# Kernel optimization log

Hardware: AMD Instinct MI355X
Metric: run time of the kernel (lower is better)

The kernel has to match this reference:

```python
import jax, jax.numpy as jnp
import numpy as np

N = 100000
E = 1600000
IN = 128
HID = 128
OUT = 64


def sage_conv(x, src, dst, deg_inv, W_l, b_l, W_r):
    # PyG SAGEConv (mean aggr): out = lin_l(mean_{j in N(i)} x_j) + lin_r(x_i)
    msgs = x[src]                                   # [E, F] gather
    agg = jax.ops.segment_sum(msgs, dst, num_segments=N)  # [N, F]
    agg = agg * deg_inv[:, None]                    # mean
    return agg @ W_l + b_l + x @ W_r


def setup_inputs() -> dict:
    key = jax.random.key(0)
    ks = jax.random.split(key, 9)
    x = jax.random.normal(ks[0], (N, IN), dtype=jnp.float32)
    edge_index = jax.random.randint(ks[1], (2, E), 0, N, dtype=jnp.int64)
    s = 1.0 / np.sqrt(IN)
    W1l = jax.random.uniform(ks[2], (IN, HID), jnp.float32, -s, s)
    b1 = jax.random.uniform(ks[3], (HID,), jnp.float32, -s, s)
    W1r = jax.random.uniform(ks[4], (IN, HID), jnp.float32, -s, s)
    s2 = 1.0 / np.sqrt(HID)
    W2l = jax.random.uniform(ks[5], (HID, HID), jnp.float32, -s2, s2)
    b2 = jax.random.uniform(ks[6], (HID,), jnp.float32, -s2, s2)
    W2r = jax.random.uniform(ks[7], (HID, HID), jnp.float32, -s2, s2)
    kl1, kl2 = jax.random.split(ks[8])
    Wlin = jax.random.uniform(kl1, (HID, OUT), jnp.float32, -s2, s2)
    blin = jax.random.uniform(kl2, (OUT,), jnp.float32, -s2, s2)
    return {"x": x, "edge_index": edge_index, "W1l": W1l, "b1": b1, "W1r": W1r,
            "W2l": W2l, "b2": b2, "W2r": W2r, "Wlin": Wlin, "blin": blin}


def reference(x, edge_index, W1l, b1, W1r, W2l, b2, W2r, Wlin, blin):
    src, dst = edge_index[0], edge_index[1]
    deg = jax.ops.segment_sum(jnp.ones((E,), jnp.float32), dst, num_segments=N)
    deg_inv = 1.0 / jnp.maximum(deg, 1.0)
    h = sage_conv(x, src, dst, deg_inv, W1l, b1, W1r)
    h = jax.nn.relu(h)
    # dropout: training=False -> identity
    h2 = sage_conv(h, src, dst, deg_inv, W2l, b2, W2r)
    h = jax.nn.relu(h + h2)
    return h @ Wlin + blin
```

## Files before the change

kernel.cpp:

```cpp
#include <hip/hip_runtime.h>
#include <hip/hip_bf16.h>
#include <cstdint>

#define NND 100000
#define NED 1600000
#define FIN 128
#define FOUT 64

#define NBLK 512
#define EPB (NED / NBLK)
#define NBUCK 256
#define BSH 9
#define BNODES 512
#define HTN (NBUCK * NBLK)

typedef __bf16 bf16x8 __attribute__((ext_vector_type(8)));
typedef float f32x4 __attribute__((ext_vector_type(4)));

static __device__ inline unsigned short f2bf(float f) {
    unsigned int u = __builtin_bit_cast(unsigned int, f);
    unsigned int r = (u + 0x7fffu + ((u >> 16) & 1u)) >> 16;
    return (unsigned short)r;
}
static __device__ inline float bflo(unsigned int v) {
    return __builtin_bit_cast(float, v << 16);
}
static __device__ inline float bfhi(unsigned int v) {
    return __builtin_bit_cast(float, v & 0xffff0000u);
}
static __device__ inline float bf1(unsigned short u) {
    return __builtin_bit_cast(float, (unsigned int)u << 16);
}

static __device__ inline void pack_one(const float* __restrict__ W,
                                       unsigned short* __restrict__ out,
                                       int NTtot, int c_local, int nt,
                                       int chunkOff, int ncols, int lane) {
    int k = c_local * 32 + (lane >> 4) * 8;
    int n = nt * 16 + (lane & 15);
    unsigned short t[8];
#pragma unroll
    for (int j = 0; j < 8; j++) t[j] = f2bf(W[(size_t)(k + j) * ncols + n]);
    uint4 u;
    u.x = t[0] | ((unsigned)t[1] << 16);
    u.y = t[2] | ((unsigned)t[3] << 16);
    u.z = t[4] | ((unsigned)t[5] << 16);
    u.w = t[6] | ((unsigned)t[7] << 16);
    *(uint4*)&out[((size_t)((c_local + chunkOff) * NTtot + nt) * 64 + lane) * 8] = u;
}

__global__ __launch_bounds__(256) void k_hist_cast(
        const int* __restrict__ dst, int* __restrict__ histT,
        const float* __restrict__ x, unsigned int* __restrict__ xb,
        const float* W1l, const float* W1r, const float* W2l,
        const float* W2r, const float* Wlin,
        unsigned short* p1, unsigned short* p2, unsigned short* ph) {
    __shared__ int hist[NBUCK];
    const int tid = threadIdx.x, blk = blockIdx.x;
    hist[tid] = 0;
    __syncthreads();
    const int e0 = blk * EPB, e1 = e0 + EPB;
    for (int i = e0 + tid; i < e1; i += 256)
        atomicAdd(&hist[dst[i] >> BSH], 1);
    __syncthreads();
    histT[tid * NBLK + blk] = hist[tid];
    if (blk < 144 && tid < 64) {
        int b = blk, lane = tid;
        if (b < 32)       pack_one(W1l, p1, 8, b >> 3, b & 7, 0, 128, lane);
        else if (b < 64)  { b -= 32; pack_one(W1r, p1, 8, b >> 3, b & 7, 4, 128, lane); }
        else if (b < 96)  { b -= 64; pack_one(W2l, p2, 8, b >> 3, b & 7, 0, 128, lane); }
        else if (b < 128) { b -= 96; pack_one(W2r, p2, 8, b >> 3, b & 7, 4, 128, lane); }
        else              { b -= 128; pack_one(Wlin, ph, 4, b >> 2, b & 3, 0, 64, lane); }
    }
    const int total2 = NND * 64;
    for (int i = blk * 256 + tid; i < total2; i += NBLK * 256) {
        float2 v = ((const float2*)x)[i];
        xb[i] = (unsigned int)f2bf(v.x) | ((unsigned int)f2bf(v.y) << 16);
    }
}

__global__ __launch_bounds__(1024) void g_scan1(const int* __restrict__ in,
                                                int* __restrict__ psum, int n) {
    __shared__ int red[1024];
    int tid = threadIdx.x;
    int i = blockIdx.x * 1024 + tid;
    red[tid] = (i < n) ? in[i] : 0;
    __syncthreads();
#pragma unroll
    for (int off = 512; off > 0; off >>= 1) {
        if (tid < off) red[tid] += red[tid + off];
        __syncthreads();
    }
    if (tid == 0) psum[blockIdx.x] = red[0];
}

__global__ __launch_bounds__(128) void g_scan2(int* __restrict__ psum, int nb) {
    int tid = threadIdx.x;
    int d = (tid < nb) ? psum[tid] : 0;
    int v = d;
#pragma unroll
    for (int off = 1; off < 64; off <<= 1) {
        int u = __shfl_up(v, off, 64);
        if ((tid & 63) >= off) v += u;
    }
    __shared__ int ws[2];
    if ((tid & 63) == 63) ws[tid >> 6] = v;
    __syncthreads();
    int base = (tid >= 64) ? ws[0] : 0;
    if (tid < nb) psum[tid] = base + v - d;
}

__global__ __launch_bounds__(1024) void g_scan3(const int* __restrict__ in,
                                                const int* __restrict__ psum,
                                                int* __restrict__ out, int n) {
    int tid = threadIdx.x;
    int i = blockIdx.x * 1024 + tid;
    int d = (i < n) ? in[i] : 0;
    int v = d;
#pragma unroll
    for (int off = 1; off < 64; off <<= 1) {
        int u = __shfl_up(v, off, 64);
        if ((tid & 63) >= off) v += u;
    }
    __shared__ int wsum[16];
    int wid = tid >> 6;
    if ((tid & 63) == 63) wsum[wid] = v;
    __syncthreads();
    if (tid < 16) {
        int w = wsum[tid];
#pragma unroll
        for (int off = 1; off < 16; off <<= 1) {
            int u = __shfl_up(w, off, 64);
            if (tid >= off) w += u;
        }
        wsum[tid] = w;
    }
    __syncthreads();
    int base = psum[blockIdx.x] + (wid ? wsum[wid - 1] : 0);
    if (i < n) out[i] = base + v - d;
}

__global__ __launch_bounds__(256) void k_scatter(const int* __restrict__ src,
                                                 const int* __restrict__ dst,
                                                 const int* __restrict__ sh,
                                                 uint2* __restrict__ eS) {
    __shared__ int cur[NBUCK];
    const int tid = threadIdx.x, blk = blockIdx.x;
    cur[tid] = sh[tid * NBLK + blk];
    __syncthreads();
    const int e0 = blk * EPB, e1 = e0 + EPB;
    for (int i = e0 + tid; i < e1; i += 256) {
        int d = dst[i];
        int pos = atomicAdd(&cur[d >> BSH], 1);
        eS[pos] = make_uint2((unsigned)src[i], (unsigned)(d & (BNODES - 1)));
    }
}

__global__ __launch_bounds__(1024) void k_bucket(const uint2* __restrict__ eS,
                                                 const int* __restrict__ sh,
                                                 int* __restrict__ csr,
                                                 int* __restrict__ offs,
                                                 float* __restrict__ dinv, int n) {
    __shared__ int cnt[BNODES];
    __shared__ int loc[BNODES];
    const int b = blockIdx.x, tid = threadIdx.x;
    const int base = sh[b * NBLK];
    const int end = (b == NBUCK - 1) ? NED : sh[(b + 1) * NBLK];
    if (tid < BNODES) cnt[tid] = 0;
    __syncthreads();
    for (int i = base + tid; i < end; i += 1024)
        atomicAdd(&cnt[eS[i].y], 1);
    __syncthreads();
    if (tid < BNODES) loc[tid] = cnt[tid];
    __syncthreads();
#pragma unroll
    for (int off = 1; off < BNODES; off <<= 1) {
        int v = 0;
        if (tid < BNODES && tid >= off) v = loc[tid - off];
        __syncthreads();
        if (tid < BNODES) loc[tid] += v;
        __syncthreads();
    }
    int node = b * BNODES + tid;
    int myExcl = 0;
    if (tid < BNODES) {
        myExcl = loc[tid] - cnt[tid];
        if (node < n) {
            offs[node] = base + myExcl;
            dinv[node] = 1.0f / fmaxf((float)cnt[tid], 1.0f);
        }
    }
    __syncthreads();
    if (tid < BNODES) cnt[tid] = base + myExcl;
    __syncthreads();
    for (int i = base + tid; i < end; i += 1024) {
        uint2 e = eS[i];
        int slot = atomicAdd(&cnt[e.y], 1);
        csr[slot] = (int)e.x;
    }
    if (b == 0 && tid == 0) offs[n] = NED;
}

#define ACC8(v) do { \
    acc[0].x += bflo((v).x); acc[0].y += bfhi((v).x); \
    acc[1].x += bflo((v).y); acc[1].y += bfhi((v).y); \
    acc[2].x += bflo((v).z); acc[2].y += bfhi((v).z); \
    acc[3].x += bflo((v).w); acc[3].y += bfhi((v).w); } while (0)

__global__ __launch_bounds__(256) void k_aggb(const uint4* __restrict__ feat4,
                                              const int* __restrict__ offs,
                                              const int* __restrict__ csr,
                                              const float* __restrict__ dinv,
                                              uint4* __restrict__ out4, int n) {
    int node = blockIdx.x * 4 + (threadIdx.x >> 6);
    if (node >= n) return;
    int lane = threadIdx.x & 63;
    int grp = lane >> 4;
    int ch = lane & 15;
    int beg = offs[node], end = offs[node + 1];
    int deg = end - beg;

    float2 acc[4];
#pragma unroll
    for (int j = 0; j < 4; j++) acc[j] = make_float2(0.f, 0.f);

    int i = beg;
    int fullEnd = beg + (deg & ~15);
    for (; i < fullEnd; i += 16) {
        int s0 = csr[i + grp];
        int s1 = csr[i + 4 + grp];
        int s2 = csr[i + 8 + grp];
        int s3 = csr[i + 12 + grp];
        uint4 v0 = feat4[(size_t)s0 * 16 + ch];
        uint4 v1 = feat4[(size_t)s1 * 16 + ch];
        uint4 v2 = feat4[(size_t)s2 * 16 + ch];
        uint4 v3 = feat4[(size_t)s3 * 16 + ch];
        ACC8(v0); ACC8(v1); ACC8(v2); ACC8(v3);
    }
    if (i < end) {
#pragma unroll
        for (int g = 0; g < 4; g++) {
            int e = i + g * 4 + grp;
            bool p = e < end;
            int s = csr[p ? e : beg];
            uint4 v = feat4[(size_t)s * 16 + ch];
            if (p) { ACC8(v); }
        }
    }
#pragma unroll
    for (int j = 0; j < 4; j++) {
        acc[j].x += __shfl_xor(acc[j].x, 16);
        acc[j].y += __shfl_xor(acc[j].y, 16);
        acc[j].x += __shfl_xor(acc[j].x, 32);
        acc[j].y += __shfl_xor(acc[j].y, 32);
    }
    if (grp == 0) {
        float di = dinv[node];
        uint4 o;
        o.x = (unsigned)f2bf(acc[0].x * di) | ((unsigned)f2bf(acc[0].y * di) << 16);
        o.y = (unsigned)f2bf(acc[1].x * di) | ((unsigned)f2bf(acc[1].y * di) << 16);
        o.z = (unsigned)f2bf(acc[2].x * di) | ((unsigned)f2bf(acc[2].y * di) << 16);
        o.w = (unsigned)f2bf(acc[3].x * di) | ((unsigned)f2bf(acc[3].y * di) << 16);
        out4[(size_t)node * 16 + ch] = o;
    }
}

template <int NT, int KCH, bool TWO, bool RELU, bool RESID, bool HEAD, bool OUTBF>
__global__ __launch_bounds__(256) void k_mfma(const unsigned short* __restrict__ P,
                                              const unsigned short* __restrict__ Q,
                                              const unsigned short* __restrict__ Wp,
                                              const float* __restrict__ bias,
                                              const unsigned short* __restrict__ resid,
                                              const unsigned short* __restrict__ Wp2,
                                              const float* __restrict__ bias2,
                                              void* __restrict__ outv, int n) {
    const int lane = threadIdx.x & 63;
    const int wave = threadIdx.x >> 6;
    const int quad = lane >> 4;
    const int row0 = blockIdx.x * 64 + wave * 16;
    int rowA = row0 + (lane & 15);
    if (rowA >= n) rowA = n - 1;

    f32x4 acc[NT];
#pragma unroll
    for (int t = 0; t < NT; t++) acc[t] = (f32x4){0.f, 0.f, 0.f, 0.f};

#pragma unroll
    for (int c = 0; c < KCH; c++) {
        const unsigned short* Abase = (TWO && c >= KCH / 2) ? Q : P;
        const int kk = (TWO ? (c & (KCH / 2 - 1)) : c) * 32 + quad * 8;
        bf16x8 a = *(const bf16x8*)&Abase[(size_t)rowA * 128 + kk];
#pragma unroll
        for (int t = 0; t < NT; t++) {
            bf16x8 b = *(const bf16x8*)&Wp[(size_t)((c * NT + t) * 64 + lane) * 8];
            acc[t] = __builtin_amdgcn_mfma_f32_16x16x32_bf16(a, b, acc[t], 0, 0, 0);
        }
    }

    const int col = lane & 15;
    if (!HEAD) {
#pragma unroll
        for (int t = 0; t < NT; t++) {
            float bv = bias[t * 16 + col];
#pragma unroll
            for (int r = 0; r < 4; r++) {
                int row = row0 + quad * 4 + r;
                if (row < n) {
                    float v = acc[t][r] + bv;
                    if (RESID) v += bf1(resid[(size_t)row * 128 + t * 16 + col]);
                    if (RELU) v = fmaxf(v, 0.f);
                    if (OUTBF)
                        ((unsigned short*)outv)[(size_t)row * (NT * 16) + t * 16 + col] = f2bf(v);
                    else
                        ((float*)outv)[(size_t)row * (NT * 16) + t * 16 + col] = v;
                }
            }
        }
    } else {
        __shared__ __align__(16) unsigned short sT[4][16 * 136];
#pragma unroll
        for (int t = 0; t < NT; t++) {
            float bv = bias[t * 16 + col];
#pragma unroll
            for (int r = 0; r < 4; r++) {
                int row = row0 + quad * 4 + r;
                int rr = row < n ? row : n - 1;
                float v = acc[t][r] + bv;
                if (RESID) v += bf1(resid[(size_t)rr * 128 + t * 16 + col]);
                if (RELU) v = fmaxf(v, 0.f);
                sT[wave][(quad * 4 + r) * 136 + t * 16 + col] = f2bf(v);
            }
        }
        f32x4 hacc[4];
#pragma unroll
        for (int t = 0; t < 4; t++) hacc[t] = (f32x4){0.f, 0.f, 0.f, 0.f};
#pragma unroll
        for (int c = 0; c < 4; c++) {
            bf16x8 a = *(const bf16x8*)&sT[wave][(lane & 15) * 136 + c * 32 + quad * 8];
#pragma unroll
            for (int t = 0; t < 4; t++) {
                bf16x8 b = *(const bf16x8*)&Wp2[(size_t)((c * 4 + t) * 64 + lane) * 8];
                hacc[t] = __builtin_amdgcn_mfma_f32_16x16x32_bf16(a, b, hacc[t], 0, 0, 0);
            }
        }
#pragma unroll
        for (int t = 0; t < 4; t++) {
            float bv = bias2[t * 16 + col];
#pragma unroll
            for (int r = 0; r < 4; r++) {
                int row = row0 + quad * 4 + r;
                if (row < n)
                    ((float*)outv)[(size_t)row * 64 + t * 16 + col] = hacc[t][r] + bv;
            }
        }
    }
}

extern "C" void kernel_launch(void* const* d_in, const int* in_sizes, int n_in,
                              void* d_out, int out_size, void* d_ws, size_t ws_size,
                              hipStream_t stream) {
    const float* x    = (const float*)d_in[0];
    const int*   ei   = (const int*)d_in[1];
    const float* W1l  = (const float*)d_in[2];
    const float* b1   = (const float*)d_in[3];
    const float* W1r  = (const float*)d_in[4];
    const float* W2l  = (const float*)d_in[5];
    const float* b2   = (const float*)d_in[6];
    const float* W2r  = (const float*)d_in[7];
    const float* Wlin = (const float*)d_in[8];
    const float* blin = (const float*)d_in[9];
    float* out = (float*)d_out;

    const int N = NND, E = NED;
    const int* src = ei;
    const int* dst = ei + E;
    const int NB2 = HTN / 1024;

    char* w = (char*)d_ws;
    int*   histT  = (int*)w;               w += (size_t)HTN * 4;
    int*   sh     = (int*)w;               w += (size_t)HTN * 4;
    int*   psum   = (int*)w;               w += (size_t)NB2 * 4;
    int*   offs   = (int*)w;               w += (size_t)(N + 4) * 4;
    float* dinv   = (float*)w;             w += (size_t)N * 4;
    uint2* eS     = (uint2*)w;             w += (size_t)E * 8;
    int*   csr    = (int*)w;               w += (size_t)E * 4;
    unsigned short* p1  = (unsigned short*)w;  w += 256 * 128 * 2;
    unsigned short* p2  = (unsigned short*)w;  w += 256 * 128 * 2;
    unsigned short* ph  = (unsigned short*)w;  w += 128 * 64 * 2;
    unsigned short* xb  = (unsigned short*)w;  w += (size_t)N * 128 * 2;
    unsigned short* agg = (unsigned short*)w;  w += (size_t)N * 128 * 2;
    unsigned short* h1  = (unsigned short*)w;  w += (size_t)N * 128 * 2;

    k_hist_cast<<<NBLK, 256, 0, stream>>>(dst, histT, x, (unsigned int*)xb,
                                          W1l, W1r, W2l, W2r, Wlin, p1, p2, ph);
    g_scan1<<<NB2, 1024, 0, stream>>>(histT, psum, HTN);
    g_scan2<<<1, 128, 0, stream>>>(psum, NB2);
    g_scan3<<<NB2, 1024, 0, stream>>>(histT, psum, sh, HTN);
    k_scatter<<<NBLK, 256, 0, stream>>>(src, dst, sh, eS);
    k_bucket<<<NBUCK, 1024, 0, stream>>>(eS, sh, csr, offs, dinv, N);

    k_aggb<<<(N + 3) / 4, 256, 0, stream>>>((const uint4*)xb, offs, csr, dinv,
                                            (uint4*)agg, N);
    k_mfma<8, 8, true, true, false, false, true><<<(N + 63) / 64, 256, 0, stream>>>(
        agg, xb, p1, b1, nullptr, nullptr, nullptr, h1, N);

    k_aggb<<<(N + 3) / 4, 256, 0, stream>>>((const uint4*)h1, offs, csr, dinv,
                                            (uint4*)agg, N);
    k_mfma<8, 8, true, true, true, true, false><<<(N + 63) / 64, 256, 0, stream>>>(
        agg, h1, p2, b2, h1, ph, blin, out, N);
}
```

Measured before the change: 388.0 us.

## Process two nodes per wave in aggregation and two row tiles per MFMA wave

The aggregation kernel now has each wave handle two destination nodes at once, interleaving their neighbor gathers so more loads are in flight per wave. The MFMA kernels give each wave 32 rows instead of 16, so every weight fragment load feeds two MFMAs. The cast of x to bf16 now uses float4 loads. The cost is more registers and fewer, larger blocks, which may lower occupancy. Load balance can also suffer when the two paired nodes have different degrees.

Result: slower. 438.4 us (+13.0%).

```diff
diff --git a/kernel.cpp b/kernel.cpp
--- a/kernel.cpp
+++ b/kernel.cpp
@@ -72,10 +72,13 @@
         else if (b < 128) { b -= 96; pack_one(W2r, p2, 8, b >> 3, b & 7, 4, 128, lane); }
         else              { b -= 128; pack_one(Wlin, ph, 4, b >> 2, b & 3, 0, 64, lane); }
     }
-    const int total2 = NND * 64;
-    for (int i = blk * 256 + tid; i < total2; i += NBLK * 256) {
-        float2 v = ((const float2*)x)[i];
-        xb[i] = (unsigned int)f2bf(v.x) | ((unsigned int)f2bf(v.y) << 16);
+    const int total4 = NND * 32;
+    for (int i = blk * 256 + tid; i < total4; i += NBLK * 256) {
+        float4 v = ((const float4*)x)[i];
+        uint2 o;
+        o.x = (unsigned)f2bf(v.x) | ((unsigned)f2bf(v.y) << 16);
+        o.y = (unsigned)f2bf(v.z) | ((unsigned)f2bf(v.w) << 16);
+        ((uint2*)xb)[i] = o;
     }
 }
 
@@ -201,67 +204,116 @@
     if (b == 0 && tid == 0) offs[n] = NED;
 }
 
-#define ACC8(v) do { \
-    acc[0].x += bflo((v).x); acc[0].y += bfhi((v).x); \
-    acc[1].x += bflo((v).y); acc[1].y += bfhi((v).y); \
-    acc[2].x += bflo((v).z); acc[2].y += bfhi((v).z); \
-    acc[3].x += bflo((v).w); acc[3].y += bfhi((v).w); } while (0)
+#define ACCP(A, v) do { \
+    A[0].x += bflo((v).x); A[0].y += bfhi((v).x); \
+    A[1].x += bflo((v).y); A[1].y += bfhi((v).y); \
+    A[2].x += bflo((v).z); A[2].y += bfhi((v).z); \
+    A[3].x += bflo((v).w); A[3].y += bfhi((v).w); } while (0)
 
 __global__ __launch_bounds__(256) void k_aggb(const uint4* __restrict__ feat4,
                                               const int* __restrict__ offs,
                                               const int* __restrict__ csr,
                                               const float* __restrict__ dinv,
                                               uint4* __restrict__ out4, int n) {
-    int node = blockIdx.x * 4 + (threadIdx.x >> 6);
-    if (node >= n) return;
-    int lane = threadIdx.x & 63;
-    int grp = lane >> 4;
-    int ch = lane & 15;
-    int beg = offs[node], end = offs[node + 1];
-    int deg = end - beg;
-
-    float2 acc[4];
-#pragma unroll
-    for (int j = 0; j < 4; j++) acc[j] = make_float2(0.f, 0.f);
-
-    int i = beg;
-    int fullEnd = beg + (deg & ~15);
-    for (; i < fullEnd; i += 16) {
-        int s0 = csr[i + grp];
-        int s1 = csr[i + 4 + grp];
-        int s2 = csr[i + 8 + grp];
-        int s3 = csr[i + 12 + grp];
+    const int wid = blockIdx.x * 4 + (threadIdx.x >> 6);
+    const int nodeA = wid * 2;
+    if (nodeA >= n) return;
+    const int nodeB = nodeA + 1;
+    const bool hasB = nodeB < n;
+    const int lane = threadIdx.x & 63;
+    const int grp = lane >> 4;
+    const int ch = lane & 15;
+
+    const int begA = offs[nodeA];
+    const int endA = offs[nodeA + 1];
+    const int begB = hasB ? offs[nodeB] : 0;
+    const int endB = hasB ? offs[nodeB + 1] : 0;
+
+    float2 accA[4], accB[4];
+#pragma unroll
+    for (int j = 0; j < 4; j++) {
+        accA[j] = make_float2(0.f, 0.f);
+        accB[j] = make_float2(0.f, 0.f);
+    }
+
+    int iA = begA, iB = begB;
+    const int fullA = begA + ((endA - begA) & ~15);
+    const int fullB = begB + ((endB - begB) & ~15);
+
+    while (iA < fullA && iB < fullB) {
+        int sa0 = csr[iA + grp], sa1 = csr[iA + 4 + grp];
+        int sa2 = csr[iA + 8 + grp], sa3 = csr[iA + 12 + grp];
+        int sb0 = csr[iB + grp], sb1 = csr[iB + 4 + grp];
+        int sb2 = csr[iB + 8 + grp], sb3 = csr[iB + 12 + grp];
+        uint4 va0 = feat4[(size_t)sa0 * 16 + ch];
+        uint4 va1 = feat4[(size_t)sa1 * 16 + ch];
+        uint4 va2 = feat4[(size_t)sa2 * 16 + ch];
+        uint4 va3 = feat4[(size_t)sa3 * 16 + ch];
+        uint4 vb0 = feat4[(size_t)sb0 * 16 + ch];
+        uint4 vb1 = feat4[(size_t)sb1 * 16 + ch];
+        uint4 vb2 = feat4[(size_t)sb2 * 16 + ch];
+        uint4 vb3 = feat4[(size_t)sb3 * 16 + ch];
+        ACCP(accA, va0); ACCP(accA, va1); ACCP(accA, va2); ACCP(accA, va3);
+        ACCP(accB, vb0); ACCP(accB, vb1); ACCP(accB, vb2); ACCP(accB, vb3);
+        iA += 16; iB += 16;
+    }
+    for (; iA < fullA; iA += 16) {
+        int s0 = csr[iA + grp], s1 = csr[iA + 4 + grp];
+        int s2 = csr[iA + 8 + grp], s3 = csr[iA + 12 + grp];
         uint4 v0 = feat4[(size_t)s0 * 16 + ch];
         uint4 v1 = feat4[(size_t)s1 * 16 + ch];
         uint4 v2 = feat4[(size_t)s2 * 16 + ch];
         uint4 v3 = feat4[(size_t)s3 * 16 + ch];
-        ACC8(v0); ACC8(v1); ACC8(v2); ACC8(v3);
-    }
-    if (i < end) {
-#pragma unroll
-        for (int g = 0; g < 4; g++) {
-            int e = i + g * 4 + grp;
-            bool p = e < end;
-            int s = csr[p ? e : beg];
-            uint4 v = feat4[(size_t)s * 16 + ch];
-            if (p) { ACC8(v); }
-        }
+        ACCP(accA, v0); ACCP(accA, v1); ACCP(accA, v2); ACCP(accA, v3);
+    }
+    for (; iB < fullB; iB += 16) {
+        int s0 = csr[iB + grp], s1 = csr[iB + 4 + grp];
+        int s2 = csr[iB + 8 + grp], s3 = csr[iB + 12 + grp];
+        uint4 v0 = feat4[(size_t)s0 * 16 + ch];
+        uint4 v1 = feat4[(size_t)s1 * 16 + ch];
+        uint4 v2 = feat4[(size_t)s2 * 16 + ch];
+        uint4 v3 = feat4[(size_t)s3 * 16 + ch];
+        ACCP(accB, v0); ACCP(accB, v1); ACCP(accB, v2); ACCP(accB, v3);
+    }
+#pragma unroll
+    for (int g = 0; g < 4; g++) {
+        int eA = iA + g * 4 + grp;
+        int eB = iB + g * 4 + grp;
+        uint4 vA = make_uint4(0u, 0u, 0u, 0u);
+        uint4 vB = make_uint4(0u, 0u, 0u, 0u);
+        if (eA < endA) vA = feat4[(size_t)csr[eA] * 16 + ch];
+        if (eB < endB) vB = feat4[(size_t)csr[eB] * 16 + ch];
+        ACCP(accA, vA);
+        ACCP(accB, vB);
     }
 #pragma unroll
     for (int j = 0; j < 4; j++) {
-        acc[j].x += __shfl_xor(acc[j].x, 16);
-        acc[j].y += __shfl_xor(acc[j].y, 16);
-        acc[j].x += __shfl_xor(acc[j].x, 32);
-        acc[j].y += __shfl_xor(acc[j].y, 32);
+        accA[j].x += __shfl_xor(accA[j].x, 16);
+        accA[j].y += __shfl_xor(accA[j].y, 16);
+        accA[j].x += __shfl_xor(accA[j].x, 32);
+        accA[j].y += __shfl_xor(accA[j].y, 32);
+        accB[j].x += __shfl_xor(accB[j].x, 16);
+        accB[j].y += __shfl_xor(accB[j].y, 16);
+        accB[j].x += __shfl_xor(accB[j].x, 32);
+        accB[j].y += __shfl_xor(accB[j].y, 32);
     }
     if (grp == 0) {
-        float di = dinv[node];
+        float di = dinv[nodeA];
         uint4 o;
-        o.x = (unsigned)f2bf(acc[0].x * di) | ((unsigned)f2bf(acc[0].y * di) << 16);
-        o.y = (unsigned)f2bf(acc[1].x * di) | ((unsigned)f2bf(acc[1].y * di) << 16);
-        o.z = (unsigned)f2bf(acc[2].x * di) | ((unsigned)f2bf(acc[2].y * di) << 16);
-        o.w = (unsigned)f2bf(acc[3].x * di) | ((unsigned)f2bf(acc[3].y * di) << 16);
-        out4[(size_t)node * 16 + ch] = o;
+        o.x = (unsigned)f2bf(accA[0].x * di) | ((unsigned)f2bf(accA[0].y * di) << 16);
+        o.y = (unsigned)f2bf(accA[1].x * di) | ((unsigned)f2bf(accA[1].y * di) << 16);
+        o.z = (unsigned)f2bf(accA[2].x * di) | ((unsigned)f2bf(accA[2].y * di) << 16);
+        o.w = (unsigned)f2bf(accA[3].x * di) | ((unsigned)f2bf(accA[3].y * di) << 16);
+        out4[(size_t)nodeA * 16 + ch] = o;
+        if (hasB) {
+            float d2 = dinv[nodeB];
+            uint4 p;
+            p.x = (unsigned)f2bf(accB[0].x * d2) | ((unsigned)f2bf(accB[0].y * d2) << 16);
+            p.y = (unsigned)f2bf(accB[1].x * d2) | ((unsigned)f2bf(accB[1].y * d2) << 16);
+            p.z = (unsigned)f2bf(accB[2].x * d2) | ((unsigned)f2bf(accB[2].y * d2) << 16);
+            p.w = (unsigned)f2bf(accB[3].x * d2) | ((unsigned)f2bf(accB[3].y * d2) << 16);
+            out4[(size_t)nodeB * 16 + ch] = p;
+        }
     }
 }
 
@@ -277,23 +329,30 @@
     const int lane = threadIdx.x & 63;
     const int wave = threadIdx.x >> 6;
     const int quad = lane >> 4;
-    const int row0 = blockIdx.x * 64 + wave * 16;
-    int rowA = row0 + (lane & 15);
-    if (rowA >= n) rowA = n - 1;
-
-    f32x4 acc[NT];
-#pragma unroll
-    for (int t = 0; t < NT; t++) acc[t] = (f32x4){0.f, 0.f, 0.f, 0.f};
+    const int row0 = blockIdx.x * 128 + wave * 32;
+    int rA0 = row0 + (lane & 15);
+    if (rA0 >= n) rA0 = n - 1;
+    int rA1 = row0 + 16 + (lane & 15);
+    if (rA1 >= n) rA1 = n - 1;
+
+    f32x4 acc0[NT], acc1[NT];
+#pragma unroll
+    for (int t = 0; t < NT; t++) {
+        acc0[t] = (f32x4){0.f, 0.f, 0.f, 0.f};
+        acc1[t] = (f32x4){0.f, 0.f, 0.f, 0.f};
+    }
 
 #pragma unroll
     for (int c = 0; c < KCH; c++) {
         const unsigned short* Abase = (TWO && c >= KCH / 2) ? Q : P;
         const int kk = (TWO ? (c & (KCH / 2 - 1)) : c) * 32 + quad * 8;
-        bf16x8 a = *(const bf16x8*)&Abase[(size_t)rowA * 128 + kk];
+        bf16x8 a0 = *(const bf16x8*)&Abase[(size_t)rA0 * 128 + kk];
+        bf16x8 a1 = *(const bf16x8*)&Abase[(size_t)rA1 * 128 + kk];
 #pragma unroll
         for (int t = 0; t < NT; t++) {
             bf16x8 b = *(const bf16x8*)&Wp[(size_t)((c * NT + t) * 64 + lane) * 8];
-            acc[t] = __builtin_amdgcn_mfma_f32_16x16x32_bf16(a, b, acc[t], 0, 0, 0);
+            acc0[t] = __builtin_amdgcn_mfma_f32_16x16x32_bf16(a0, b, acc0[t], 0, 0, 0);
+            acc1[t] = __builtin_amdgcn_mfma_f32_16x16x32_bf16(a1, b, acc1[t], 0, 0, 0);
         }
     }
 
@@ -303,54 +362,69 @@
         for (int t = 0; t < NT; t++) {
             float bv = bias[t * 16 + col];
 #pragma unroll
-            for (int r = 0; r < 4; r++) {
-                int row = row0 + quad * 4 + r;
-                if (row < n) {
-                    float v = acc[t][r] + bv;
-                    if (RESID) v += bf1(resid[(size_t)row * 128 + t * 16 + col]);
-                    if (RELU) v = fmaxf(v, 0.f);
-                    if (OUTBF)
-                        ((unsigned short*)outv)[(size_t)row * (NT * 16) + t * 16 + col] = f2bf(v);
-                    else
-                        ((float*)outv)[(size_t)row * (NT * 16) + t * 16 + col] = v;
+            for (int h = 0; h < 2; h++) {
+#pragma unroll
+                for (int r = 0; r < 4; r++) {
+                    int row = row0 + h * 16 + quad * 4 + r;
+                    if (row < n) {
+                        float v = (h ? acc1[t][r] : acc0[t][r]) + bv;
+                        if (RESID) v += bf1(resid[(size_t)row * 128 + t * 16 + col]);
+                        if (RELU) v = fmaxf(v, 0.f);
+                        if (OUTBF)
+                            ((unsigned short*)outv)[(size_t)row * (NT * 16) + t * 16 + col] = f2bf(v);
+                        else
+                            ((float*)outv)[(size_t)row * (NT * 16) + t * 16 + col] = v;
+                    }
                 }
             }
         }
     } else {
-        __shared__ __align__(16) unsigned short sT[4][16 * 136];
+        __shared__ __align__(16) unsigned short sT[4][32 * 136];
 #pragma unroll
         for (int t = 0; t < NT; t++) {
             float bv = bias[t * 16 + col];
 #pragma unroll
-            for (int r = 0; r < 4; r++) {
-                int row = row0 + quad * 4 + r;
-                int rr = row < n ? row : n - 1;
-                float v = acc[t][r] + bv;
-                if (RESID) v += bf1(resid[(size_t)rr * 128 + t * 16 + col]);
-                if (RELU) v = fmaxf(v, 0.f);
-                sT[wave][(quad * 4 + r) * 136 + t * 16 + col] = f2bf(v);
+            for (int h = 0; h < 2; h++) {
+#pragma unroll
+                for (int r = 0; r < 4; r++) {
+                    int row = row0 + h * 16 + quad * 4 + r;
+                    int rr = row < n ? row : n - 1;
+                    float v = (h ? acc1[t][r] : acc0[t][r]) + bv;
+                    if (RESID) v += bf1(resid[(size_t)rr * 128 + t * 16 + col]);
+                    if (RELU) v = fmaxf(v, 0.f);
+                    sT[wave][(h * 16 + quad * 4 + r) * 136 + t * 16 + col] = f2bf(v);
+                }
             }
         }
-        f32x4 hacc[4];
-#pragma unroll
-        for (int t = 0; t < 4; t++) hacc[t] = (f32x4){0.f, 0.f, 0.f, 0.f};
+        f32x4 hacc0[4], hacc1[4];
+#pragma unroll
+        for (int t = 0; t < 4; t++) {
+            hacc0[t] = (f32x4){0.f, 0.f, 0.f, 0.f};
+            hacc1[t] = (f32x4){0.f, 0.f, 0.f, 0.f};
+        }
 #pragma unroll
         for (int c = 0; c < 4; c++) {
-            bf16x8 a = *(const bf16x8*)&sT[wave][(lane & 15) * 136 + c * 32 + quad * 8];
+            bf16x8 a0 = *(const bf16x8*)&sT[wave][(lane & 15) * 136 + c * 32 + quad * 8];
+            bf16x8 a1 = *(const bf16x8*)&sT[wave][((lane & 15) + 16) * 136 + c * 32 + quad * 8];
 #pragma unroll
             for (int t = 0; t < 4; t++) {
                 bf16x8 b = *(const bf16x8*)&Wp2[(size_t)((c * 4 + t) * 64 + lane) * 8];
-                hacc[t] = __builtin_amdgcn_mfma_f32_16x16x32_bf16(a, b, hacc[t], 0, 0, 0);
+                hacc0[t] = __builtin_amdgcn_mfma_f32_16x16x32_bf16(a0, b, hacc0[t], 0, 0, 0);
+                hacc1[t] = __builtin_amdgcn_mfma_f32_16x16x32_bf16(a1, b, hacc1[t], 0, 0, 0);
             }
         }
 #pragma unroll
         for (int t = 0; t < 4; t++) {
             float bv = bias2[t * 16 + col];
 #pragma unroll
-            for (int r = 0; r < 4; r++) {
-                int row = row0 + quad * 4 + r;
-                if (row < n)
-                    ((float*)outv)[(size_t)row * 64 + t * 16 + col] = hacc[t][r] + bv;
+            for (int h = 0; h < 2; h++) {
+#pragma unroll
+                for (int r = 0; r < 4; r++) {
+                    int row = row0 + h * 16 + quad * 4 + r;
+                    if (row < n)
+                        ((float*)outv)[(size_t)row * 64 + t * 16 + col] =
+                            (h ? hacc1[t][r] : hacc0[t][r]) + bv;
+                }
             }
         }
     }
@@ -399,13 +473,13 @@
     k_scatter<<<NBLK, 256, 0, stream>>>(src, dst, sh, eS);
     k_bucket<<<NBUCK, 1024, 0, stream>>>(eS, sh, csr, offs, dinv, N);
 
-    k_aggb<<<(N + 3) / 4, 256, 0, stream>>>((const uint4*)xb, offs, csr, dinv,
+    k_aggb<<<(N + 7) / 8, 256, 0, stream>>>((const uint4*)xb, offs, csr, dinv,
                                             (uint4*)agg, N);
-    k_mfma<8, 8, true, true, false, false, true><<<(N + 63) / 64, 256, 0, stream>>>(
+    k_mfma<8, 8, true, true, false, false, true><<<(N + 127) / 128, 256, 0, stream>>>(
         agg, xb, p1, b1, nullptr, nullptr, nullptr, h1, N);
 
-    k_aggb<<<(N + 3) / 4, 256, 0, stream>>>((const uint4*)h1, offs, csr, dinv,
+    k_aggb<<<(N + 7) / 8, 256, 0, stream>>>((const uint4*)h1, offs, csr, dinv,
                                             (uint4*)agg, N);
-    k_mfma<8, 8, true, true, true, true, false><<<(N + 63) / 64, 256, 0, stream>>>(
+    k_mfma<8, 8, true, true, true, true, false><<<(N + 127) / 128, 256, 0, stream>>>(
         agg, h1, p2, b2, h1, ph, blin, out, N);
 }
```

## Slice node features into 16-column planes for cache-local aggregation

Applied to the files above, without the earlier changes.

Stores bf16 node features in a sliced layout of 8 planes, each [N][16], and launches the aggregation kernel as a persistent grid. The block index sets the slice, so concurrently running blocks gather from a 3.2 MB plane that can stay cache-resident. The MFMA kernels' loads, residual reads and stores are rewritten to index the sliced layout. In exchange, each wave now gathers only 32-byte chunks per neighbour, so every slice re-reads the CSR indices, and the per-node loop becomes serial over 16-edge chunks.

Result: slower. 578.0 us (+49.0%).

```diff
diff --git a/kernel.cpp b/kernel.cpp
--- a/kernel.cpp
+++ b/kernel.cpp
@@ -13,6 +13,9 @@
 #define BSH 9
 #define BNODES 512
 #define HTN (NBUCK * NBLK)
+
+#define NSLICE 8
+#define AGGC 2048
 
 typedef __bf16 bf16x8 __attribute__((ext_vector_type(8)));
 typedef float f32x4 __attribute__((ext_vector_type(4)));
@@ -72,10 +75,17 @@
         else if (b < 128) { b -= 96; pack_one(W2r, p2, 8, b >> 3, b & 7, 4, 128, lane); }
         else              { b -= 128; pack_one(Wlin, ph, 4, b >> 2, b & 3, 0, 64, lane); }
     }
-    const int total2 = NND * 64;
-    for (int i = blk * 256 + tid; i < total2; i += NBLK * 256) {
-        float2 v = ((const float2*)x)[i];
-        xb[i] = (unsigned int)f2bf(v.x) | ((unsigned int)f2bf(v.y) << 16);
+    const int total = NND * 32;
+    for (int j = blk * 256 + tid; j < total; j += NBLK * 256) {
+        int sNode = j >> 2;
+        int part = j & 3;
+        int s = sNode / NND;
+        int node = sNode - s * NND;
+        float4 v = ((const float4*)x)[node * 32 + s * 4 + part];
+        uint2 o;
+        o.x = (unsigned)f2bf(v.x) | ((unsigned)f2bf(v.y) << 16);
+        o.y = (unsigned)f2bf(v.z) | ((unsigned)f2bf(v.w) << 16);
+        ((uint2*)xb)[j] = o;
     }
 }
 
@@ -201,67 +211,52 @@
     if (b == 0 && tid == 0) offs[n] = NED;
 }
 
-#define ACC8(v) do { \
-    acc[0].x += bflo((v).x); acc[0].y += bfhi((v).x); \
-    acc[1].x += bflo((v).y); acc[1].y += bfhi((v).y); \
-    acc[2].x += bflo((v).z); acc[2].y += bfhi((v).z); \
-    acc[3].x += bflo((v).w); acc[3].y += bfhi((v).w); } while (0)
-
-__global__ __launch_bounds__(256) void k_aggb(const uint4* __restrict__ feat4,
+__global__ __launch_bounds__(256) void k_aggb(const unsigned short* __restrict__ featS,
                                               const int* __restrict__ offs,
                                               const int* __restrict__ csr,
                                               const float* __restrict__ dinv,
-                                              uint4* __restrict__ out4, int n) {
-    int node = blockIdx.x * 4 + (threadIdx.x >> 6);
-    if (node >= n) return;
-    int lane = threadIdx.x & 63;
-    int grp = lane >> 4;
-    int ch = lane & 15;
-    int beg = offs[node], end = offs[node + 1];
-    int deg = end - beg;
-
-    float2 acc[4];
-#pragma unroll
-    for (int j = 0; j < 4; j++) acc[j] = make_float2(0.f, 0.f);
-
-    int i = beg;
-    int fullEnd = beg + (deg & ~15);
-    for (; i < fullEnd; i += 16) {
-        int s0 = csr[i + grp];
-        int s1 = csr[i + 4 + grp];
-        int s2 = csr[i + 8 + grp];
-        int s3 = csr[i + 12 + grp];
-        uint4 v0 = feat4[(size_t)s0 * 16 + ch];
-        uint4 v1 = feat4[(size_t)s1 * 16 + ch];
-        uint4 v2 = feat4[(size_t)s2 * 16 + ch];
-        uint4 v3 = feat4[(size_t)s3 * 16 + ch];
-        ACC8(v0); ACC8(v1); ACC8(v2); ACC8(v3);
-    }
-    if (i < end) {
-#pragma unroll
-        for (int g = 0; g < 4; g++) {
-            int e = i + g * 4 + grp;
-            bool p = e < end;
-            int s = csr[p ? e : beg];
-            uint4 v = feat4[(size_t)s * 16 + ch];
-            if (p) { ACC8(v); }
-        }
-    }
-#pragma unroll
-    for (int j = 0; j < 4; j++) {
-        acc[j].x += __shfl_xor(acc[j].x, 16);
-        acc[j].y += __shfl_xor(acc[j].y, 16);
-        acc[j].x += __shfl_xor(acc[j].x, 32);
-        acc[j].y += __shfl_xor(acc[j].y, 32);
-    }
-    if (grp == 0) {
-        float di = dinv[node];
-        uint4 o;
-        o.x = (unsigned)f2bf(acc[0].x * di) | ((unsigned)f2bf(acc[0].y * di) << 16);
-        o.y = (unsigned)f2bf(acc[1].x * di) | ((unsigned)f2bf(acc[1].y * di) << 16);
-        o.z = (unsigned)f2bf(acc[2].x * di) | ((unsigned)f2bf(acc[2].y * di) << 16);
-        o.w = (unsigned)f2bf(acc[3].x * di) | ((unsigned)f2bf(acc[3].y * di) << 16);
-        out4[(size_t)node * 16 + ch] = o;
+                                              unsigned short* __restrict__ outS, int n) {
+    const int s = blockIdx.x & 7;
+    const int wid0 = (blockIdx.x >> 3) * 4 + (threadIdx.x >> 6);
+    const int lane = threadIdx.x & 63;
+    const int g = lane >> 2;
+    const int q = lane & 3;
+    const uint2* fS = (const uint2*)featS + (size_t)s * n * 4;
+    uint2* oS = (uint2*)outS + (size_t)s * n * 4;
+
+    for (int node = wid0; node < n; node += AGGC * 4) {
+        const int beg = offs[node], end = offs[node + 1];
+        const int deg = end - beg;
+        const int full = beg + (deg & ~15);
+        f32x4 acc = (f32x4){0.f, 0.f, 0.f, 0.f};
+        {
+            int e = full + g;
+            if (e < end) {
+                uint2 v = fS[(size_t)csr[e] * 4 + q];
+                acc.x += bflo(v.x); acc.y += bfhi(v.x);
+                acc.z += bflo(v.y); acc.w += bfhi(v.y);
+            }
+        }
+        for (int i = beg; i < full; i += 16) {
+            int s0 = csr[i + g];
+            uint2 v = fS[(size_t)s0 * 4 + q];
+            acc.x += bflo(v.x); acc.y += bfhi(v.x);
+            acc.z += bflo(v.y); acc.w += bfhi(v.y);
+        }
+#pragma unroll
+        for (int m = 4; m <= 32; m <<= 1) {
+            acc.x += __shfl_xor(acc.x, m);
+            acc.y += __shfl_xor(acc.y, m);
+            acc.z += __shfl_xor(acc.z, m);
+            acc.w += __shfl_xor(acc.w, m);
+        }
+        if (g == 0) {
+            float di = dinv[node];
+            uint2 o;
+            o.x = (unsigned)f2bf(acc.x * di) | ((unsigned)f2bf(acc.y * di) << 16);
+            o.y = (unsigned)f2bf(acc.z * di) | ((unsigned)f2bf(acc.w * di) << 16);
+            oS[(size_t)node * 4 + q] = o;
+        }
     }
 }
 
@@ -289,7 +284,7 @@
     for (int c = 0; c < KCH; c++) {
         const unsigned short* Abase = (TWO && c >= KCH / 2) ? Q : P;
         const int kk = (TWO ? (c & (KCH / 2 - 1)) : c) * 32 + quad * 8;
-        bf16x8 a = *(const bf16x8*)&Abase[(size_t)rowA * 128 + kk];
+        bf16x8 a = *(const bf16x8*)&Abase[((size_t)(kk >> 4) * NND + rowA) * 16 + (kk & 15)];
 #pragma unroll
         for (int t = 0; t < NT; t++) {
             bf16x8 b = *(const bf16x8*)&Wp[(size_t)((c * NT + t) * 64 + lane) * 8];
@@ -307,10 +302,10 @@
                 int row = row0 + quad * 4 + r;
                 if (row < n) {
                     float v = acc[t][r] + bv;
-                    if (RESID) v += bf1(resid[(size_t)row * 128 + t * 16 + col]);
+                    if (RESID) v += bf1(resid[((size_t)t * NND + row) * 16 + col]);
                     if (RELU) v = fmaxf(v, 0.f);
                     if (OUTBF)
-                        ((unsigned short*)outv)[(size_t)row * (NT * 16) + t * 16 + col] = f2bf(v);
+                        ((unsigned short*)outv)[((size_t)t * NND + row) * 16 + col] = f2bf(v);
                     else
                         ((float*)outv)[(size_t)row * (NT * 16) + t * 16 + col] = v;
                 }
@@ -326,7 +321,7 @@
                 int row = row0 + quad * 4 + r;
                 int rr = row < n ? row : n - 1;
                 float v = acc[t][r] + bv;
-                if (RESID) v += bf1(resid[(size_t)rr * 128 + t * 16 + col]);
+                if (RESID) v += bf1(resid[((size_t)t * NND + rr) * 16 + col]);
                 if (RELU) v = fmaxf(v, 0.f);
                 sT[wave][(quad * 4 + r) * 136 + t * 16 + col] = f2bf(v);
             }
@@ -399,13 +394,11 @@
     k_scatter<<<NBLK, 256, 0, stream>>>(src, dst, sh, eS);
     k_bucket<<<NBUCK, 1024, 0, stream>>>(eS, sh, csr, offs, dinv, N);
 
-    k_aggb<<<(N + 3) / 4, 256, 0, stream>>>((const uint4*)xb, offs, csr, dinv,
-                                            (uint4*)agg, N);
+    k_aggb<<<AGGC * 8, 256, 0, stream>>>(xb, offs, csr, dinv, agg, N);
     k_mfma<8, 8, true, true, false, false, true><<<(N + 63) / 64, 256, 0, stream>>>(
         agg, xb, p1, b1, nullptr, nullptr, nullptr, h1, N);
 
-    k_aggb<<<(N + 3) / 4, 256, 0, stream>>>((const uint4*)h1, offs, csr, dinv,
-                                            (uint4*)agg, N);
+    k_aggb<<<AGGC * 8, 256, 0, stream>>>(h1, offs, csr, dinv, agg, N);
     k_mfma<8, 8, true, true, true, true, false><<<(N + 63) / 64, 256, 0, stream>>>(
         agg, h1, p2, b2, h1, ph, blin, out, N);
 }
```
